# Performance work log

Measured on AMD Instinct MI355X. Metric: run time of the kernel, lower is better.

Reference implementation:

```python
import jax, jax.numpy as jnp
import numpy as np

DIM = 1024
MLP_MULT = 4
NUM_EXPERTS = 8
EXPERT_HIDDEN = MLP_MULT * DIM // NUM_EXPERTS  # 512


def setup_inputs() -> dict:
    key = jax.random.key(0)
    k_x, k_r, k_fc, k_pj = jax.random.split(key, 4)
    x = jax.random.normal(k_x, (4, 4096, DIM), dtype=jnp.float32)
    # router: nn.Linear(dim, num_experts, bias=False) -> weight [E, D]
    w_router = jax.random.normal(k_r, (NUM_EXPERTS, DIM), dtype=jnp.float32) * (1.0 / np.sqrt(DIM))
    # per-expert fc: Linear(dim, hidden) weight [H, D]; stacked [E, H, D]
    w_fc = jax.random.normal(k_fc, (NUM_EXPERTS, EXPERT_HIDDEN, DIM), dtype=jnp.float32) * (1.0 / np.sqrt(DIM))
    # per-expert proj: Linear(hidden, dim) weight [D, H]; stacked [E, D, H]
    # (_zero_init in the original; use small random values so the reference output is non-trivial)
    w_proj = jax.random.normal(k_pj, (NUM_EXPERTS, DIM, EXPERT_HIDDEN), dtype=jnp.float32) * (1.0 / np.sqrt(EXPERT_HIDDEN))
    return {"x": x, "w_router": w_router, "w_fc": w_fc, "w_proj": w_proj}


def reference(x, w_router, w_fc, w_proj):
    # Router on detached input; top-1 expert per token.
    logits = jnp.einsum('bsd,ed->bse', jax.lax.stop_gradient(x), w_router)
    weights = jax.nn.softmax(logits, axis=-1)  # computed as in original (unused in output)
    indices = jnp.argmax(weights, axis=-1)     # [B, S]
    onehot = jax.nn.one_hot(indices, NUM_EXPERTS, dtype=x.dtype)  # [B, S, E]
    # Dense dispatch: run all experts, combine with one-hot (equivalent to mask gather/scatter).
    h = jnp.einsum('bsd,ehd->bseh', x, w_fc)              # [B, S, E, H]
    h = jnp.where(h >= 0, h, 0.5 * h)                      # leaky_relu(negative_slope=0.5)
    h = h * h                                              # square
    out = jnp.einsum('bseh,edh,bse->bsd', h, w_proj, onehot)
    return out
```

## Files before the change

### kernel.cpp

```cpp
#include <hip/hip_runtime.h>
#include <stdint.h>
#include <stddef.h>

#define DIM 1024
#define NEXP 8
#define HID 512
#define NTOK 16384
#define NB_HIST 64
#define NB_ROUTER 1024
#define NB_CAST 512

typedef __attribute__((ext_vector_type(4))) float f32x4;
typedef __attribute__((ext_vector_type(8))) short short8;
typedef __attribute__((ext_vector_type(4))) unsigned short u16x4;

__device__ __forceinline__ unsigned short f2b(float f) {
  unsigned int u = __float_as_uint(f);
  return (unsigned short)((u + 0x7FFFu + ((u >> 16) & 1u)) >> 16);
}

__device__ __forceinline__ void gload_lds16(const unsigned short* g, unsigned short* l) {
  __builtin_amdgcn_global_load_lds((const __attribute__((address_space(1))) void*)g,
                                   (__attribute__((address_space(3))) void*)l, 16, 0, 0);
}

__global__ __launch_bounds__(256) void k_router_cast(
    const float* __restrict__ x, const float* __restrict__ wr,
    int* __restrict__ eid, unsigned short* __restrict__ xb,
    const float* __restrict__ wfc, const float* __restrict__ wpj,
    unsigned short* __restrict__ oa, unsigned short* __restrict__ ob) {
  int bid = blockIdx.x;
  if (bid < NB_ROUTER) {
    int w = threadIdx.x >> 6, lane = threadIdx.x & 63;
    int t0 = bid * 16 + w * 4;
    const float* xr = x + (size_t)t0 * DIM;
    unsigned short* xbr = xb + (size_t)t0 * DIM;
    float s[4][NEXP];
#pragma unroll
    for (int j = 0; j < 4; j++)
#pragma unroll
      for (int e = 0; e < NEXP; e++) s[j][e] = 0.f;
#pragma unroll
    for (int i = 0; i < 4; i++) {
      f32x4 xv[4];
#pragma unroll
      for (int j = 0; j < 4; j++) {
        xv[j] = *(const f32x4*)(xr + j * DIM + lane * 4 + 256 * i);
        u16x4 u;
        u.x = f2b(xv[j].x); u.y = f2b(xv[j].y); u.z = f2b(xv[j].z); u.w = f2b(xv[j].w);
        *(u16x4*)(xbr + j * DIM + lane * 4 + 256 * i) = u;
      }
#pragma unroll
      for (int e = 0; e < NEXP; e++) {
        f32x4 wv = *(const f32x4*)(wr + e * DIM + lane * 4 + 256 * i);
#pragma unroll
        for (int j = 0; j < 4; j++)
          s[j][e] += xv[j].x * wv.x + xv[j].y * wv.y + xv[j].z * wv.z + xv[j].w * wv.w;
      }
    }
#pragma unroll
    for (int j = 0; j < 4; j++)
#pragma unroll
      for (int e = 0; e < NEXP; e++) {
        float v = s[j][e];
#pragma unroll
        for (int off = 32; off > 0; off >>= 1) v += __shfl_xor(v, off);
        s[j][e] = v;
      }
    if (lane == 0) {
#pragma unroll
      for (int j = 0; j < 4; j++) {
        int be = 0;
        float bv = s[j][0];
#pragma unroll
        for (int e = 1; e < NEXP; e++) {
          if (s[j][e] > bv) { bv = s[j][e]; be = e; }
        }
        eid[t0 + j] = be;
      }
    }
  } else {
    const int n4 = NEXP * HID * DIM / 4;
    int stride = NB_CAST * 256;
    for (int i = (bid - NB_ROUTER) * 256 + (int)threadIdx.x; i < n4; i += stride) {
      f32x4 va = ((const f32x4*)wfc)[i];
      f32x4 vb = ((const f32x4*)wpj)[i];
      u16x4 ua, ub;
      ua.x = f2b(va.x); ua.y = f2b(va.y); ua.z = f2b(va.z); ua.w = f2b(va.w);
      ub.x = f2b(vb.x); ub.y = f2b(vb.y); ub.z = f2b(vb.z); ub.w = f2b(vb.w);
      ((u16x4*)oa)[i] = ua;
      ((u16x4*)ob)[i] = ub;
    }
  }
}

__global__ __launch_bounds__(256) void k_hist(const int* __restrict__ eid,
                                              int* __restrict__ bc) {
  __shared__ int h[NEXP];
  if (threadIdx.x < NEXP) h[threadIdx.x] = 0;
  __syncthreads();
  int tok = blockIdx.x * (NTOK / NB_HIST) + threadIdx.x;
  atomicAdd(&h[eid[tok]], 1);
  __syncthreads();
  if (threadIdx.x < NEXP) bc[blockIdx.x * NEXP + threadIdx.x] = h[threadIdx.x];
}

__global__ void k_scan(const int* __restrict__ bc, int* __restrict__ offs,
                       int* __restrict__ base) {
  __shared__ int cnt[NEXP];
  __shared__ int so[NEXP + 1];
  int t = threadIdx.x;
  if (t < NEXP) {
    int run = 0;
    for (int b = 0; b < NB_HIST; b++) {
      base[b * NEXP + t] = run;
      run += bc[b * NEXP + t];
    }
    cnt[t] = run;
  }
  __syncthreads();
  if (t == 0) {
    int a = 0;
    for (int e = 0; e < NEXP; e++) { so[e] = a; a += cnt[e]; }
    so[NEXP] = a;
  }
  __syncthreads();
  if (t < NEXP + 1) offs[t] = so[t];
  for (int i = t; i < NB_HIST * NEXP; i += blockDim.x) base[i] += so[i % NEXP];
}

__global__ __launch_bounds__(256) void k_scatter(const int* __restrict__ eid,
                                                 const int* __restrict__ base,
                                                 int* __restrict__ tlist) {
  __shared__ int cur[NEXP];
  if (threadIdx.x < NEXP) cur[threadIdx.x] = base[blockIdx.x * NEXP + threadIdx.x];
  __syncthreads();
  int tok = blockIdx.x * (NTOK / NB_HIST) + threadIdx.x;
  int e = eid[tok];
  int pos = atomicAdd(&cur[e], 1);
  tlist[pos] = tok;
}

template <int KDIM, int NDIM, int NB, bool IS_FC>
__global__ __launch_bounds__(256) void k_gemm(
    const unsigned short* __restrict__ xb, const unsigned short* __restrict__ hin,
    const unsigned short* __restrict__ wb, const int* __restrict__ offs,
    const int* __restrict__ tlist, unsigned short* __restrict__ hout,
    float* __restrict__ out) {
  int l = ((int)blockIdx.x & 7) * ((int)gridDim.x >> 3) + ((int)blockIdx.x >> 3);
  int e = -1, mb = 0, nb = 0, acc2 = 0;
#pragma unroll
  for (int i = 0; i < NEXP; i++) {
    int mi = offs[i + 1] - offs[i];
    int tb = ((mi + 127) >> 7) * NB;
    if (e < 0 && l < acc2 + tb) {
      int r = l - acc2;
      e = i; mb = r / NB; nb = r % NB;
    }
    acc2 += tb;
  }
  if (e < 0) return;
  int off = offs[e];
  int me = offs[e + 1] - off;
  int m0 = mb * 128;
  int n0 = nb * 128;

  __shared__ unsigned short lds[3][2][128 * 32];

  int t = threadIdx.x;
  int lane = t & 63, w = t >> 6;
  int wm = w >> 1, wn = w & 1;

  int kb = (lane & 3) ^ ((lane >> 2) & 3);

  const unsigned short* asrc[2];
  const unsigned short* bsrc[2];
#pragma unroll
  for (int i = 0; i < 2; i++) {
    int r = i * 64 + w * 16 + (lane >> 2);
    int gm = m0 + r;
    if (gm > me - 1) gm = me - 1;
    if (IS_FC) {
      int tok = tlist[off + gm];
      asrc[i] = xb + (size_t)tok * KDIM + kb * 8;
    } else {
      asrc[i] = hin + (size_t)(off + gm) * KDIM + kb * 8;
    }
    bsrc[i] = wb + ((size_t)e * NDIM + n0 + r) * (size_t)KDIM + kb * 8;
  }

  f32x4 acc[4][4] = {};
  const int NT = KDIM / 32;

  unsigned short* b0a = &lds[0][0][0]; unsigned short* b0b = &lds[0][1][0];
  unsigned short* b1a = &lds[1][0][0]; unsigned short* b1b = &lds[1][1][0];
  unsigned short* b2a = &lds[2][0][0]; unsigned short* b2b = &lds[2][1][0];

#define STAGE(kt_, da_, db_)                                   \
  do {                                                         \
    gload_lds16(asrc[0] + (kt_) * 32, (da_) + (w * 16) * 32);  \
    gload_lds16(asrc[1] + (kt_) * 32, (da_) + (64 + w * 16) * 32); \
    gload_lds16(bsrc[0] + (kt_) * 32, (db_) + (w * 16) * 32);  \
    gload_lds16(bsrc[1] + (kt_) * 32, (db_) + (64 + w * 16) * 32); \
  } while (0)

  STAGE(0, b0a, b0b);
  STAGE(1, b1a, b1b);

  for (int kt = 0; kt < NT; kt++) {
    if (kt < NT - 1) {
      asm volatile("s_waitcnt vmcnt(4)" ::: "memory");
    } else {
      asm volatile("s_waitcnt vmcnt(0)" ::: "memory");
    }
    __builtin_amdgcn_s_barrier();

    if (kt + 2 < NT) STAGE(kt + 2, b2a, b2b);

    short8 af[4], bf[4];
#pragma unroll
    for (int i = 0; i < 4; i++) {
      int ra = wm * 64 + i * 16 + (lane & 15);
      int ca = (lane >> 4) ^ (ra & 3);
      af[i] = *(const short8*)&b0a[ra * 32 + ca * 8];
      int rb = wn * 64 + i * 16 + (lane & 15);
      int cb = (lane >> 4) ^ (rb & 3);
      bf[i] = *(const short8*)&b0b[rb * 32 + cb * 8];
    }
    __builtin_amdgcn_s_setprio(1);
#pragma unroll
    for (int mi = 0; mi < 4; mi++)
#pragma unroll
      for (int ni = 0; ni < 4; ni++)
        acc[mi][ni] =
            __builtin_amdgcn_mfma_f32_16x16x32_bf16(af[mi], bf[ni], acc[mi][ni], 0, 0, 0);
    __builtin_amdgcn_s_setprio(0);

    unsigned short* ta = b0a; b0a = b1a; b1a = b2a; b2a = ta;
    unsigned short* tb = b0b; b0b = b1b; b1b = b2b; b2b = tb;
  }
#undef STAGE

  int rb = (lane >> 4) * 4, cb = lane & 15;
#pragma unroll
  for (int mi = 0; mi < 4; mi++) {
#pragma unroll
    for (int j = 0; j < 4; j++) {
      int ml = wm * 64 + mi * 16 + rb + j;
      if (m0 + ml < me) {
        if (IS_FC) {
#pragma unroll
          for (int ni = 0; ni < 4; ni++) {
            int col = n0 + wn * 64 + ni * 16 + cb;
            float v = acc[mi][ni][j];
            v = (v >= 0.f) ? v * v : 0.25f * v * v;
            hout[(size_t)(off + m0 + ml) * HID + col] = f2b(v);
          }
        } else {
          int tok = tlist[off + m0 + ml];
#pragma unroll
          for (int ni = 0; ni < 4; ni++) {
            int col = n0 + wn * 64 + ni * 16 + cb;
            out[(size_t)tok * DIM + col] = acc[mi][ni][j];
          }
        }
      }
    }
  }
}

extern "C" void kernel_launch(void* const* d_in, const int* in_sizes, int n_in,
                              void* d_out, int out_size, void* d_ws, size_t ws_size,
                              hipStream_t stream) {
  const float* x = (const float*)d_in[0];
  const float* wr = (const float*)d_in[1];
  const float* wfc = (const float*)d_in[2];
  const float* wpj = (const float*)d_in[3];
  float* out = (float*)d_out;

  uintptr_t p = (uintptr_t)d_ws;
  int* offs = (int*)p;  p += 256;
  int* bc = (int*)p;    p += sizeof(int) * NB_HIST * NEXP;
  int* base = (int*)p;  p += sizeof(int) * NB_HIST * NEXP;
  int* eid = (int*)p;   p += sizeof(int) * NTOK;
  int* tlist = (int*)p; p += sizeof(int) * NTOK;
  unsigned short* wfc_b = (unsigned short*)p; p += (size_t)NEXP * HID * DIM * 2;
  unsigned short* wpj_b = (unsigned short*)p; p += (size_t)NEXP * DIM * HID * 2;
  unsigned short* hbuf = (unsigned short*)p;  p += (size_t)NTOK * HID * 2;
  unsigned short* xb = (unsigned short*)p;    p += (size_t)NTOK * DIM * 2;

  k_router_cast<<<NB_ROUTER + NB_CAST, 256, 0, stream>>>(
      x, wr, eid, xb, wfc, wpj, wfc_b, wpj_b);
  k_hist<<<NB_HIST, 256, 0, stream>>>(eid, bc);
  k_scan<<<1, 256, 0, stream>>>(bc, offs, base);
  k_scatter<<<NB_HIST, 256, 0, stream>>>(eid, base, tlist);
  k_gemm<1024, 512, 4, true><<<dim3(544), 256, 0, stream>>>(
      xb, nullptr, wfc_b, offs, tlist, hbuf, nullptr);
  k_gemm<512, 1024, 8, false><<<dim3(1080), 256, 0, stream>>>(
      nullptr, hbuf, wpj_b, offs, tlist, nullptr, out);
}
```

Before: 111.3 us.

## Fuse x bf16 cast into FC GEMM A-tile loads and change LDS swizzle

Drops the separate bf16 copy of x that the router kernel wrote. The FC GEMM now loads fp32 token rows directly, converts them to bf16 in registers and writes them to LDS, while weights still use direct global-to-LDS loads. This removes a 32 MB write and a 32 MB reread of xb. In exchange, the FC kernel reads twice the A bytes per tile and adds conversion ALU work plus LDS stores inside the pipeline. The LDS bank swizzle is also changed to use bits 3-4 of the lane and bits 1-2 of the row, in both GEMMs.

```diff
diff --git a/kernel.cpp b/kernel.cpp
--- a/kernel.cpp
+++ b/kernel.cpp
@@ -13,6 +13,7 @@
 typedef __attribute__((ext_vector_type(4))) float f32x4;
 typedef __attribute__((ext_vector_type(8))) short short8;
 typedef __attribute__((ext_vector_type(4))) unsigned short u16x4;
+typedef __attribute__((ext_vector_type(8))) unsigned short u16x8;
 
 __device__ __forceinline__ unsigned short f2b(float f) {
   unsigned int u = __float_as_uint(f);
@@ -26,7 +27,7 @@
 
 __global__ __launch_bounds__(256) void k_router_cast(
     const float* __restrict__ x, const float* __restrict__ wr,
-    int* __restrict__ eid, unsigned short* __restrict__ xb,
+    int* __restrict__ eid,
     const float* __restrict__ wfc, const float* __restrict__ wpj,
     unsigned short* __restrict__ oa, unsigned short* __restrict__ ob) {
   int bid = blockIdx.x;
@@ -34,7 +35,6 @@
     int w = threadIdx.x >> 6, lane = threadIdx.x & 63;
     int t0 = bid * 16 + w * 4;
     const float* xr = x + (size_t)t0 * DIM;
-    unsigned short* xbr = xb + (size_t)t0 * DIM;
     float s[4][NEXP];
 #pragma unroll
     for (int j = 0; j < 4; j++)
@@ -44,12 +44,7 @@
     for (int i = 0; i < 4; i++) {
       f32x4 xv[4];
 #pragma unroll
-      for (int j = 0; j < 4; j++) {
-        xv[j] = *(const f32x4*)(xr + j * DIM + lane * 4 + 256 * i);
-        u16x4 u;
-        u.x = f2b(xv[j].x); u.y = f2b(xv[j].y); u.z = f2b(xv[j].z); u.w = f2b(xv[j].w);
-        *(u16x4*)(xbr + j * DIM + lane * 4 + 256 * i) = u;
-      }
+      for (int j = 0; j < 4; j++) xv[j] = *(const f32x4*)(xr + j * DIM + lane * 4 + 256 * i);
 #pragma unroll
       for (int e = 0; e < NEXP; e++) {
         f32x4 wv = *(const f32x4*)(wr + e * DIM + lane * 4 + 256 * i);
@@ -141,14 +136,11 @@
   tlist[pos] = tok;
 }
 
-template <int KDIM, int NDIM, int NB, bool IS_FC>
-__global__ __launch_bounds__(256) void k_gemm(
-    const unsigned short* __restrict__ xb, const unsigned short* __restrict__ hin,
-    const unsigned short* __restrict__ wb, const int* __restrict__ offs,
-    const int* __restrict__ tlist, unsigned short* __restrict__ hout,
-    float* __restrict__ out) {
+__device__ __forceinline__ bool tile_map(const int* offs, int NB, int& e, int& mb,
+                                         int& nb) {
   int l = ((int)blockIdx.x & 7) * ((int)gridDim.x >> 3) + ((int)blockIdx.x >> 3);
-  int e = -1, mb = 0, nb = 0, acc2 = 0;
+  e = -1; mb = 0; nb = 0;
+  int acc2 = 0;
 #pragma unroll
   for (int i = 0; i < NEXP; i++) {
     int mi = offs[i + 1] - offs[i];
@@ -159,19 +151,149 @@
     }
     acc2 += tb;
   }
-  if (e < 0) return;
-  int off = offs[e];
-  int me = offs[e + 1] - off;
-  int m0 = mb * 128;
-  int n0 = nb * 128;
+  return e >= 0;
+}
+
+__global__ __launch_bounds__(256) void k_gemm_fc(
+    const float* __restrict__ x, const unsigned short* __restrict__ wb,
+    const int* __restrict__ offs, const int* __restrict__ tlist,
+    unsigned short* __restrict__ hout) {
+  constexpr int KDIM = DIM, NDIM = HID;
+  int e, mb, nb;
+  if (!tile_map(offs, 4, e, mb, nb)) return;
+  int off = offs[e], me = offs[e + 1] - off, m0 = mb * 128, n0 = nb * 128;
+
+  __shared__ unsigned short As[3][128 * 32];
+  __shared__ unsigned short Bs[3][128 * 32];
+
+  int t = threadIdx.x, lane = t & 63, w = t >> 6;
+  int wm = w >> 1, wn = w & 1;
+
+  int kb = (lane & 3) ^ ((lane >> 3) & 3);
+
+  const unsigned short* bsrc[2];
+  const float* af32[2];
+#pragma unroll
+  for (int i = 0; i < 2; i++) {
+    int r = i * 64 + w * 16 + (lane >> 2);
+    bsrc[i] = wb + ((size_t)e * NDIM + n0 + r) * (size_t)KDIM + kb * 8;
+    int gm = m0 + r;
+    if (gm > me - 1) gm = me - 1;
+    af32[i] = x + (size_t)tlist[off + gm] * DIM + kb * 8;
+  }
+  int awoff0 = (w * 16) * 32 + lane * 8;
+  int awoff1 = (64 + w * 16) * 32 + lane * 8;
+
+  f32x4 acc[4][4] = {};
+  constexpr int NT = KDIM / 32;
+
+  unsigned short* a0 = &As[0][0]; unsigned short* b0 = &Bs[0][0];
+  unsigned short* a1 = &As[1][0]; unsigned short* b1 = &Bs[1][0];
+  unsigned short* a2 = &As[2][0]; unsigned short* b2 = &Bs[2][0];
+
+  f32x4 r00, r01, r10, r11;
+
+#define ISSUE_A(kt_)                                              \
+  do {                                                            \
+    r00 = *(const f32x4*)(af32[0] + (kt_) * 32);                  \
+    r01 = *(const f32x4*)(af32[0] + (kt_) * 32 + 4);              \
+    r10 = *(const f32x4*)(af32[1] + (kt_) * 32);                  \
+    r11 = *(const f32x4*)(af32[1] + (kt_) * 32 + 4);              \
+  } while (0)
+#define ISSUE_B(kt_, db_)                                         \
+  do {                                                            \
+    gload_lds16(bsrc[0] + (kt_) * 32, (db_) + (w * 16) * 32);     \
+    gload_lds16(bsrc[1] + (kt_) * 32, (db_) + (64 + w * 16) * 32);\
+  } while (0)
+#define WRITE_A(da_)                                              \
+  do {                                                            \
+    u16x8 c0, c1;                                                 \
+    c0[0] = f2b(r00.x); c0[1] = f2b(r00.y); c0[2] = f2b(r00.z); c0[3] = f2b(r00.w); \
+    c0[4] = f2b(r01.x); c0[5] = f2b(r01.y); c0[6] = f2b(r01.z); c0[7] = f2b(r01.w); \
+    c1[0] = f2b(r10.x); c1[1] = f2b(r10.y); c1[2] = f2b(r10.z); c1[3] = f2b(r10.w); \
+    c1[4] = f2b(r11.x); c1[5] = f2b(r11.y); c1[6] = f2b(r11.z); c1[7] = f2b(r11.w); \
+    *(u16x8*)&(da_)[awoff0] = c0;                                 \
+    *(u16x8*)&(da_)[awoff1] = c1;                                 \
+  } while (0)
+
+  ISSUE_A(0);
+  ISSUE_B(0, b0);
+  ISSUE_B(1, b1);
+
+  for (int kt = 0; kt < NT; kt++) {
+    if (kt == NT - 1) {
+      asm volatile("s_waitcnt vmcnt(0)" ::: "memory");
+    } else {
+      asm volatile("s_waitcnt vmcnt(2)" ::: "memory");
+    }
+    __builtin_amdgcn_sched_barrier(0);
+    WRITE_A(a0);
+    asm volatile("s_waitcnt lgkmcnt(0)" ::: "memory");
+    __builtin_amdgcn_sched_barrier(0);
+    __builtin_amdgcn_s_barrier();
+    if (kt + 1 < NT) ISSUE_A(kt + 1);
+    if (kt + 2 < NT) ISSUE_B(kt + 2, b2);
+
+    short8 af[4], bf[4];
+#pragma unroll
+    for (int i = 0; i < 4; i++) {
+      int ra = wm * 64 + i * 16 + (lane & 15);
+      int ca = (lane >> 4) ^ ((ra >> 1) & 3);
+      af[i] = *(const short8*)&a0[ra * 32 + ca * 8];
+      int rbb = wn * 64 + i * 16 + (lane & 15);
+      int cb = (lane >> 4) ^ ((rbb >> 1) & 3);
+      bf[i] = *(const short8*)&b0[rbb * 32 + cb * 8];
+    }
+    __builtin_amdgcn_s_setprio(1);
+#pragma unroll
+    for (int mi = 0; mi < 4; mi++)
+#pragma unroll
+      for (int ni = 0; ni < 4; ni++)
+        acc[mi][ni] =
+            __builtin_amdgcn_mfma_f32_16x16x32_bf16(af[mi], bf[ni], acc[mi][ni], 0, 0, 0);
+    __builtin_amdgcn_s_setprio(0);
+
+    unsigned short* ta = a0; a0 = a1; a1 = a2; a2 = ta;
+    unsigned short* tb = b0; b0 = b1; b1 = b2; b2 = tb;
+  }
+#undef ISSUE_A
+#undef ISSUE_B
+#undef WRITE_A
+
+  int rb = (lane >> 4) * 4, cb = lane & 15;
+#pragma unroll
+  for (int mi = 0; mi < 4; mi++) {
+#pragma unroll
+    for (int j = 0; j < 4; j++) {
+      int ml = wm * 64 + mi * 16 + rb + j;
+      if (m0 + ml < me) {
+#pragma unroll
+        for (int ni = 0; ni < 4; ni++) {
+          int col = n0 + wn * 64 + ni * 16 + cb;
+          float v = acc[mi][ni][j];
+          v = (v >= 0.f) ? v * v : 0.25f * v * v;
+          hout[(size_t)(off + m0 + ml) * HID + col] = f2b(v);
+        }
+      }
+    }
+  }
+}
+
+__global__ __launch_bounds__(256) void k_gemm_pj(
+    const unsigned short* __restrict__ hin, const unsigned short* __restrict__ wb,
+    const int* __restrict__ offs, const int* __restrict__ tlist,
+    float* __restrict__ out) {
+  constexpr int KDIM = HID, NDIM = DIM;
+  int e, mb, nb;
+  if (!tile_map(offs, 8, e, mb, nb)) return;
+  int off = offs[e], me = offs[e + 1] - off, m0 = mb * 128, n0 = nb * 128;
 
   __shared__ unsigned short lds[3][2][128 * 32];
 
-  int t = threadIdx.x;
-  int lane = t & 63, w = t >> 6;
+  int t = threadIdx.x, lane = t & 63, w = t >> 6;
   int wm = w >> 1, wn = w & 1;
 
-  int kb = (lane & 3) ^ ((lane >> 2) & 3);
+  int kb = (lane & 3) ^ ((lane >> 3) & 3);
 
   const unsigned short* asrc[2];
   const unsigned short* bsrc[2];
@@ -180,27 +302,22 @@
     int r = i * 64 + w * 16 + (lane >> 2);
     int gm = m0 + r;
     if (gm > me - 1) gm = me - 1;
-    if (IS_FC) {
-      int tok = tlist[off + gm];
-      asrc[i] = xb + (size_t)tok * KDIM + kb * 8;
-    } else {
-      asrc[i] = hin + (size_t)(off + gm) * KDIM + kb * 8;
-    }
+    asrc[i] = hin + (size_t)(off + gm) * KDIM + kb * 8;
     bsrc[i] = wb + ((size_t)e * NDIM + n0 + r) * (size_t)KDIM + kb * 8;
   }
 
   f32x4 acc[4][4] = {};
-  const int NT = KDIM / 32;
+  constexpr int NT = KDIM / 32;
 
   unsigned short* b0a = &lds[0][0][0]; unsigned short* b0b = &lds[0][1][0];
   unsigned short* b1a = &lds[1][0][0]; unsigned short* b1b = &lds[1][1][0];
   unsigned short* b2a = &lds[2][0][0]; unsigned short* b2b = &lds[2][1][0];
 
-#define STAGE(kt_, da_, db_)                                   \
-  do {                                                         \
-    gload_lds16(asrc[0] + (kt_) * 32, (da_) + (w * 16) * 32);  \
+#define STAGE(kt_, da_, db_)                                       \
+  do {                                                             \
+    gload_lds16(asrc[0] + (kt_) * 32, (da_) + (w * 16) * 32);      \
     gload_lds16(asrc[1] + (kt_) * 32, (da_) + (64 + w * 16) * 32); \
-    gload_lds16(bsrc[0] + (kt_) * 32, (db_) + (w * 16) * 32);  \
+    gload_lds16(bsrc[0] + (kt_) * 32, (db_) + (w * 16) * 32);      \
     gload_lds16(bsrc[1] + (kt_) * 32, (db_) + (64 + w * 16) * 32); \
   } while (0)
 
@@ -221,11 +338,11 @@
 #pragma unroll
     for (int i = 0; i < 4; i++) {
       int ra = wm * 64 + i * 16 + (lane & 15);
-      int ca = (lane >> 4) ^ (ra & 3);
+      int ca = (lane >> 4) ^ ((ra >> 1) & 3);
       af[i] = *(const short8*)&b0a[ra * 32 + ca * 8];
-      int rb = wn * 64 + i * 16 + (lane & 15);
-      int cb = (lane >> 4) ^ (rb & 3);
-      bf[i] = *(const short8*)&b0b[rb * 32 + cb * 8];
+      int rbb = wn * 64 + i * 16 + (lane & 15);
+      int cb = (lane >> 4) ^ ((rbb >> 1) & 3);
+      bf[i] = *(const short8*)&b0b[rbb * 32 + cb * 8];
     }
     __builtin_amdgcn_s_setprio(1);
 #pragma unroll
@@ -248,21 +365,11 @@
     for (int j = 0; j < 4; j++) {
       int ml = wm * 64 + mi * 16 + rb + j;
       if (m0 + ml < me) {
-        if (IS_FC) {
-#pragma unroll
-          for (int ni = 0; ni < 4; ni++) {
-            int col = n0 + wn * 64 + ni * 16 + cb;
-            float v = acc[mi][ni][j];
-            v = (v >= 0.f) ? v * v : 0.25f * v * v;
-            hout[(size_t)(off + m0 + ml) * HID + col] = f2b(v);
-          }
-        } else {
-          int tok = tlist[off + m0 + ml];
-#pragma unroll
-          for (int ni = 0; ni < 4; ni++) {
-            int col = n0 + wn * 64 + ni * 16 + cb;
-            out[(size_t)tok * DIM + col] = acc[mi][ni][j];
-          }
+        int tok = tlist[off + m0 + ml];
+#pragma unroll
+        for (int ni = 0; ni < 4; ni++) {
+          int col = n0 + wn * 64 + ni * 16 + cb;
+          out[(size_t)tok * DIM + col] = acc[mi][ni][j];
         }
       }
     }
@@ -287,15 +394,12 @@
   unsigned short* wfc_b = (unsigned short*)p; p += (size_t)NEXP * HID * DIM * 2;
   unsigned short* wpj_b = (unsigned short*)p; p += (size_t)NEXP * DIM * HID * 2;
   unsigned short* hbuf = (unsigned short*)p;  p += (size_t)NTOK * HID * 2;
-  unsigned short* xb = (unsigned short*)p;    p += (size_t)NTOK * DIM * 2;
 
   k_router_cast<<<NB_ROUTER + NB_CAST, 256, 0, stream>>>(
-      x, wr, eid, xb, wfc, wpj, wfc_b, wpj_b);
+      x, wr, eid, wfc, wpj, wfc_b, wpj_b);
   k_hist<<<NB_HIST, 256, 0, stream>>>(eid, bc);
   k_scan<<<1, 256, 0, stream>>>(bc, offs, base);
   k_scatter<<<NB_HIST, 256, 0, stream>>>(eid, base, tlist);
-  k_gemm<1024, 512, 4, true><<<dim3(544), 256, 0, stream>>>(
-      xb, nullptr, wfc_b, offs, tlist, hbuf, nullptr);
-  k_gemm<512, 1024, 8, false><<<dim3(1080), 256, 0, stream>>>(
-      nullptr, hbuf, wpj_b, offs, tlist, nullptr, out);
-}
+  k_gemm_fc<<<dim3(544), 256, 0, stream>>>(x, wfc_b, offs, tlist, hbuf);
+  k_gemm_pj<<<dim3(1080), 256, 0, stream>>>(hbuf, wpj_b, offs, tlist, out);
+}
```

Result: faster. 107.4 us (-3.5%).
